# Optimization experiments

Hardware: AMD Instinct MI355X
Metric: run time of the kernel (lower is better)

The kernel has to match this reference:

```python
import jax, jax.numpy as jnp
import numpy as np

# Model constants (from init_kwargs)
NF, NC, E, B = 100000, 4000, 500000, 256
D_FACT, D_COMP = 1536, 27
HIDDEN, HEADS, CPH = 128, 4, 32  # out_per_head = hidden // heads
NUM_LAYERS = 2
TIME_DIM = 8
T_SCALE = 30.0
EDGE_DIM = 2 + TIME_DIM  # [sentiment, decay, time2vec]
ATTN_SCALE = 1.0  # 1 / attn_temperature
NEG_SLOPE = 0.2


def time_edge_features(ea, lam):
    # ea: [E, 2] = [sentiment, decay]; second column in [0,1] -> decay branch
    s = jnp.clip(ea[:, 0:1], -1.0, 1.0)
    decay = jnp.clip(ea[:, 1:2], 0.0, 1.0)
    lam = jnp.maximum(lam, 1e-6)
    delta_t = -jnp.log(jnp.maximum(decay, 1e-6)) / lam
    t = jnp.log1p(jnp.maximum(delta_t, 0.0)) / T_SCALE  # [E,1]
    freqs = jnp.arange(1, TIME_DIM, dtype=ea.dtype)      # [TIME_DIM-1]
    sins = jnp.sin(t * freqs)                            # [E,TIME_DIM-1]
    return jnp.concatenate([s, decay, sins, t], axis=-1)  # [E, EDGE_DIM]


def seg_softmax(logits, seg, n):
    # logits: [E,H]; softmax over edges sharing the same destination node
    m = jax.ops.segment_max(logits, seg, num_segments=n)
    z = jnp.exp(logits - m[seg])
    den = jax.ops.segment_sum(z, seg, num_segments=n)
    return z / (den[seg] + 1e-16)


def seg_mean(x, seg, n):
    s = jax.ops.segment_sum(x, seg, num_segments=n)
    cnt = jax.ops.segment_sum(jnp.ones((x.shape[0],), x.dtype), seg, num_segments=n)
    return s / jnp.maximum(cnt, 1.0)[:, None]


def layernorm(x, g, b, eps=1e-5):
    mu = jnp.mean(x, axis=-1, keepdims=True)
    var = jnp.var(x, axis=-1, keepdims=True)
    return (x - mu) * jax.lax.rsqrt(var + eps) * g + b


def setup_inputs() -> dict:
    key = jax.random.key(0)
    ks = jax.random.split(key, 32)

    x_fact = jax.random.normal(ks[0], (NF, D_FACT), jnp.float32)
    x_company = jax.random.normal(ks[1], (NC, D_COMP), jnp.float32)
    u = jax.random.uniform(ks[2], (E, 2), jnp.float32)
    edge_attr = jnp.concatenate([u[:, 0:1] * 2.0 - 1.0, u[:, 1:2]], axis=1)
    edge_index = jnp.stack([
        jax.random.randint(ks[3], (E,), 0, NF),
        jax.random.randint(ks[4], (E,), 0, NC),
    ]).astype(jnp.int32)
    batch_fact = jnp.sort(jax.random.randint(ks[5], (NF,), 0, B)).astype(jnp.int32)
    batch_company = jnp.sort(jax.random.randint(ks[6], (NC,), 0, B)).astype(jnp.int32)

    def p(k, shape):
        return jax.random.normal(k, shape, jnp.float32) * 0.05

    inp = dict(
        x_fact=x_fact, x_company=x_company, edge_attr=edge_attr,
        edge_index=edge_index, batch_fact=batch_fact, batch_company=batch_company,
        lambda_decay=jnp.array(0.01, jnp.float32),
        Wf=p(ks[7], (D_FACT, HIDDEN)), bf=jnp.zeros((HIDDEN,), jnp.float32),
        Wc=p(ks[8], (D_COMP, HIDDEN)), bc=jnp.zeros((HIDDEN,), jnp.float32),
        Wl=p(ks[9], (NUM_LAYERS, HIDDEN, HIDDEN)), bl=jnp.zeros((NUM_LAYERS, HIDDEN), jnp.float32),
        Wr=p(ks[10], (NUM_LAYERS, HIDDEN, HIDDEN)), br=jnp.zeros((NUM_LAYERS, HIDDEN), jnp.float32),
        We=p(ks[11], (NUM_LAYERS, EDGE_DIM, HIDDEN)), be=jnp.zeros((NUM_LAYERS, HIDDEN), jnp.float32),
        att=p(ks[12], (NUM_LAYERS, HEADS, CPH)),
        bias_out=jnp.zeros((NUM_LAYERS, HIDDEN), jnp.float32),
        ln_g=jnp.ones((NUM_LAYERS, HIDDEN), jnp.float32), ln_b=jnp.zeros((NUM_LAYERS, HIDDEN), jnp.float32),
        Wg=p(ks[13], (2 * HIDDEN, 1)), bg=jnp.zeros((1,), jnp.float32),
        W1=p(ks[14], (HIDDEN, HIDDEN)), b1=jnp.zeros((HIDDEN,), jnp.float32),
        W2=p(ks[15], (HIDDEN, 1)), b2=jnp.zeros((1,), jnp.float32),
    )
    return inp


def reference(x_fact, x_company, edge_attr, edge_index, batch_fact, batch_company,
              lambda_decay, Wf, bf, Wc, bc, Wl, bl, Wr, br, We, be, att, bias_out,
              ln_g, ln_b, Wg, bg, W1, b1, W2, b2):
    src, dst = edge_index[0], edge_index[1]
    ef = time_edge_features(edge_attr, lambda_decay)          # [E, EDGE_DIM]

    # per-node-type input encoders
    hf = jax.nn.relu(x_fact @ Wf + bf)                         # [NF, H]
    hc = jax.nn.relu(x_company @ Wc + bc)                      # [NC, H]
    n_c = x_company.shape[0]

    for l in range(NUM_LAYERS):
        # GATv2 (edge-conditioned, bipartite fact->company, share_weights=False)
        gl = (hf @ Wl[l] + bl[l]).reshape(-1, HEADS, CPH)      # src transform [NF,H,C]
        gr = (hc @ Wr[l] + br[l]).reshape(-1, HEADS, CPH)      # dst transform [NC,H,C]
        ge = (ef @ We[l] + be[l]).reshape(-1, HEADS, CPH)      # edge transform [E,H,C]
        e = jax.nn.leaky_relu(gl[src] + gr[dst] + ge, NEG_SLOPE)  # [E,H,C]
        logits = jnp.einsum('ehc,hc->eh', e, att[l]) * ATTN_SCALE  # [E,H]
        alpha = seg_softmax(logits, dst, n_c)                   # scatter-softmax over dst
        msg = alpha[..., None] * gl[src]                        # [E,H,C]
        out = jax.ops.segment_sum(msg, dst, num_segments=n_c).reshape(n_c, HIDDEN) + bias_out[l]
        hc = layernorm(hc + jax.nn.relu(out), ln_g[l], ln_b[l])  # residual + post-norm

    # gated readout over graphs in batch
    pf = seg_mean(hf, batch_fact, B)                            # [B,H]
    pc = seg_mean(hc, batch_company, B)                         # [B,H]
    g = jax.nn.sigmoid(jnp.concatenate([pf, pc], axis=-1) @ Wg + bg)  # [B,1]
    h = g * pf + (1.0 - g) * pc                                 # [B,H]
    logit = jax.nn.relu(h @ W1 + b1) @ W2 + b2                  # [B,1]
    return logit
```

## Files before the change

### kernel.cpp

```cpp
#include <hip/hip_runtime.h>
#include <hip/hip_bf16.h>
#include <math.h>

#define NFAC 100000
#define NCOMP 4000
#define NEDGE 500000
#define NB 256
#define DF 1536
#define DC 27
#define H 128
#define EDIM 10
#define EDIMP 16

typedef __attribute__((ext_vector_type(8))) short short8v;
typedef __attribute__((ext_vector_type(4))) float f32x4;

#define GLOAD_LDS16(g, l)                                                              \
  __builtin_amdgcn_global_load_lds((const __attribute__((address_space(1))) unsigned int*)(g), \
                                   (__attribute__((address_space(3))) unsigned int*)(l), 16, 0, 0)

__device__ __forceinline__ float group32_sum(float v) {
#pragma unroll
  for (int m = 16; m > 0; m >>= 1) v += __shfl_xor(v, m);
  return v;
}

__device__ __forceinline__ unsigned short bf16rn(float x) {
  unsigned int u = __float_as_uint(x);
  unsigned int r = (u + 0x7fffu + ((u >> 16) & 1u)) >> 16;
  return (unsigned short)r;
}
__device__ __forceinline__ float bf16tof(unsigned short h) {
  return __uint_as_float(((unsigned int)h) << 16);
}

__global__ void k_edge_feat(const float* __restrict__ ea, const float* __restrict__ lamp,
                            float* __restrict__ ef) {
  int e = blockIdx.x * blockDim.x + threadIdx.x;
  if (e >= NEDGE) return;
  float s   = fminf(fmaxf(ea[2 * e], -1.f), 1.f);
  float dec = fminf(fmaxf(ea[2 * e + 1], 0.f), 1.f);
  float lam = fmaxf(lamp[0], 1e-6f);
  float dt  = -logf(fmaxf(dec, 1e-6f)) / lam;
  float t   = log1pf(fmaxf(dt, 0.f)) * (1.f / 30.f);
  float* o = ef + (size_t)e * EDIMP;
  o[0] = s;
  o[1] = dec;
#pragma unroll
  for (int k = 1; k < 8; k++) o[1 + k] = __sinf(t * (float)k);
  o[9] = t;
  o[10] = 0.f; o[11] = 0.f; o[12] = 0.f; o[13] = 0.f; o[14] = 0.f; o[15] = 0.f;
}

__global__ void k_hist(const int* __restrict__ dst, int* __restrict__ deg) {
  int e = blockIdx.x * blockDim.x + threadIdx.x;
  if (e < NEDGE) atomicAdd(&deg[dst[e]], 1);
}

__global__ __launch_bounds__(1024) void k_scan(const int* __restrict__ deg, int* __restrict__ off) {
  __shared__ int s[4096];
  int t = threadIdx.x;
  for (int i = t; i < 4096; i += 1024) s[i] = (i < NCOMP) ? deg[i] : 0;
  __syncthreads();
  for (int d = 1; d < 4096; d <<= 1) {
    int vals[4];
#pragma unroll
    for (int j = 0; j < 4; j++) {
      int i = t + j * 1024;
      vals[j] = (i >= d) ? s[i - d] : 0;
    }
    __syncthreads();
#pragma unroll
    for (int j = 0; j < 4; j++) {
      int i = t + j * 1024;
      s[i] += vals[j];
    }
    __syncthreads();
  }
  for (int i = t; i < 4096; i += 1024) off[i + 1] = s[i];
  if (t == 0) off[0] = 0;
}

__global__ void k_scatter(const int* __restrict__ dst, const int* __restrict__ src,
                          const int* __restrict__ off, int* __restrict__ cur,
                          int* __restrict__ eid, int* __restrict__ srcs) {
  int e = blockIdx.x * blockDim.x + threadIdx.x;
  if (e < NEDGE) {
    int d = dst[e];
    int p = atomicAdd(&cur[d], 1);
    eid[off[d] + p] = e;
    srcs[off[d] + p] = src[e];
  }
}

__global__ void k_conv_w(const float* __restrict__ W, unsigned short* __restrict__ Bh,
                         unsigned short* __restrict__ Bl, int K) {
  int i = blockIdx.x * blockDim.x + threadIdx.x;
  if (i >= K * H) return;
  int k = i >> 7, c = i & 127;
  float x = W[i];
  unsigned short h = bf16rn(x);
  unsigned short l = bf16rn(x - bf16tof(h));
  Bh[(size_t)c * K + k] = h;
  Bl[(size_t)c * K + k] = l;
}

__device__ __forceinline__ unsigned int packhi(unsigned int u1, unsigned int u0) {
  return __builtin_amdgcn_perm(u1, u0, 0x07060302u);
}

__global__ __launch_bounds__(256, 2) void k_gemm_mfma(const float* __restrict__ A,
                                                      const unsigned short* __restrict__ Bth,
                                                      const unsigned short* __restrict__ Btl,
                                                      const float* __restrict__ bias,
                                                      float* __restrict__ C, int M, int K,
                                                      int dorelu, float* __restrict__ Cpart) {
  __shared__ __align__(16) char smem[2][32768];
  int tid = threadIdx.x;
  int wave = tid >> 6, lane = tid & 63;
  int m0 = blockIdx.x * 128;
  int wm = (wave >> 1) * 64, wn = (wave & 1) * 64;
  int fr = lane & 15, fg = lane >> 4;
  int nsplit = gridDim.y;
  int Ks = K / nsplit;
  int kbeg = blockIdx.y * Ks;
  int nIter = Ks >> 5;

  f32x4 acc[4][4];
#pragma unroll
  for (int i = 0; i < 4; i++)
#pragma unroll
    for (int j = 0; j < 4; j++) acc[i][j] = (f32x4){0.f, 0.f, 0.f, 0.f};

  int a_row = (lane >> 3);
  int a_s = lane & 7;
  int b_col = (lane >> 2);
  int b_s = lane & 3;

  auto stage = [&](int buf, int k0) {
    char* base = smem[buf];
#pragma unroll
    for (int q = 0; q < 4; q++) {
      int j = wave + 4 * q;
      int row = j * 8 + a_row;
      int grow = m0 + row;
      if (grow >= M) grow = 0;
      const float* src = A + (size_t)grow * K + k0 + ((a_s ^ (row & 7)) << 2);
      GLOAD_LDS16(src, base + j * 1024);
    }
#pragma unroll
    for (int q = 0; q < 2; q++) {
      int j = wave + 4 * q;
      int col = j * 16 + b_col;
      int soff = k0 + ((b_s ^ (col & 3)) << 3);
      GLOAD_LDS16(Bth + (size_t)col * K + soff, base + 16384 + j * 1024);
      GLOAD_LDS16(Btl + (size_t)col * K + soff, base + 24576 + j * 1024);
    }
  };

  stage(0, kbeg);
  __syncthreads();

  for (int it = 0; it < nIter; ++it) {
    int cur = it & 1;
    if (it + 1 < nIter) stage(cur ^ 1, kbeg + ((it + 1) << 5));
    const char* cb = smem[cur];
    short8v ah[4], al[4];
#pragma unroll
    for (int mf = 0; mf < 4; mf++) {
      int r = wm + 16 * mf + fr;
      int s0 = (2 * fg) ^ (r & 7);
      int s1 = (2 * fg + 1) ^ (r & 7);
      float4 a0 = *(const float4*)(cb + r * 128 + s0 * 16);
      float4 a1 = *(const float4*)(cb + r * 128 + s1 * 16);
      float xs[8] = {a0.x, a0.y, a0.z, a0.w, a1.x, a1.y, a1.z, a1.w};
      unsigned int hu[8], lu[8];
#pragma unroll
      for (int j = 0; j < 8; j++) {
        unsigned int u = __float_as_uint(xs[j]);
        hu[j] = u & 0xffff0000u;
        lu[j] = __float_as_uint(xs[j] - __uint_as_float(hu[j]));
      }
      unsigned int hw[4], lw[4];
#pragma unroll
      for (int j = 0; j < 4; j++) {
        hw[j] = packhi(hu[2 * j + 1], hu[2 * j]);
        lw[j] = packhi(lu[2 * j + 1], lu[2 * j]);
      }
      ah[mf] = *(short8v*)hw;
      al[mf] = *(short8v*)lw;
    }
#pragma unroll
    for (int nf = 0; nf < 4; nf++) {
      int c = wn + 16 * nf + fr;
      int sb = fg ^ (c & 3);
      short8v bh = *(const short8v*)(cb + 16384 + c * 64 + sb * 16);
      short8v bl = *(const short8v*)(cb + 24576 + c * 64 + sb * 16);
#pragma unroll
      for (int mf = 0; mf < 4; mf++) {
        acc[mf][nf] = __builtin_amdgcn_mfma_f32_16x16x32_bf16(ah[mf], bh, acc[mf][nf], 0, 0, 0);
        acc[mf][nf] = __builtin_amdgcn_mfma_f32_16x16x32_bf16(ah[mf], bl, acc[mf][nf], 0, 0, 0);
        acc[mf][nf] = __builtin_amdgcn_mfma_f32_16x16x32_bf16(al[mf], bh, acc[mf][nf], 0, 0, 0);
      }
    }
    __syncthreads();
  }

  if (nsplit == 1) {
#pragma unroll
    for (int mf = 0; mf < 4; mf++) {
      int rbase = m0 + wm + 16 * mf + 4 * fg;
#pragma unroll
      for (int nf = 0; nf < 4; nf++) {
        int col = wn + 16 * nf + fr;
        float bv = bias[col];
#pragma unroll
        for (int j = 0; j < 4; j++) {
          int row = rbase + j;
          if (row < M) {
            float v = acc[mf][nf][j] + bv;
            if (dorelu) v = fmaxf(v, 0.f);
            C[(size_t)row * H + col] = v;
          }
        }
      }
    }
  } else {
    float* P = Cpart + (size_t)blockIdx.y * M * H;
#pragma unroll
    for (int mf = 0; mf < 4; mf++) {
      int rbase = m0 + wm + 16 * mf + 4 * fg;
#pragma unroll
      for (int nf = 0; nf < 4; nf++) {
        int col = wn + 16 * nf + fr;
#pragma unroll
        for (int j = 0; j < 4; j++) {
          int row = rbase + j;
          if (row < M) P[(size_t)row * H + col] = acc[mf][nf][j];
        }
      }
    }
  }
}

__global__ __launch_bounds__(256) void k_reduce2(const float* __restrict__ P0,
                                                 const float* __restrict__ P1,
                                                 const float* __restrict__ bias,
                                                 float* __restrict__ C, int total4) {
  int i = blockIdx.x * blockDim.x + threadIdx.x;
  if (i >= total4) return;
  float4 a = ((const float4*)P0)[i];
  float4 b = ((const float4*)P1)[i];
  float4 bv = ((const float4*)bias)[i & 31];
  float4 r;
  r.x = fmaxf(a.x + b.x + bv.x, 0.f);
  r.y = fmaxf(a.y + b.y + bv.y, 0.f);
  r.z = fmaxf(a.z + b.z + bv.z, 0.f);
  r.w = fmaxf(a.w + b.w + bv.w, 0.f);
  ((float4*)C)[i] = r;
}

__global__ void k_enc_comp(const float* __restrict__ X, const float* __restrict__ Wc,
                           const float* __restrict__ bc, float* __restrict__ hc) {
  int tid = threadIdx.x;
  int r = blockIdx.x * 2 + (tid >> 7);
  int j = tid & 127;
  if (r >= NCOMP) return;
  float acc = bc[j];
  const float* x = X + (size_t)r * DC;
#pragma unroll
  for (int k = 0; k < DC; k++) acc = fmaf(x[k], Wc[k * H + j], acc);
  hc[(size_t)r * H + j] = fmaxf(acc, 0.f);
}

__global__ __launch_bounds__(128) void k_node(
    const float* __restrict__ gl, const float* __restrict__ ef, const int* __restrict__ srcs,
    const int* __restrict__ csr_off, const int* __restrict__ csr_eid,
    const float* __restrict__ Wr, const float* __restrict__ br, const float* __restrict__ We,
    const float* __restrict__ be, const float* __restrict__ att,
    const float* __restrict__ bias_out, const float* __restrict__ lng,
    const float* __restrict__ lnb, float* __restrict__ hc) {
  int v = blockIdx.x;
  int t = threadIdx.x;
  __shared__ float hcs[H];
  __shared__ float red[2], redq[2];
  float x = hc[(size_t)v * H + t];
  hcs[t] = x;
  float wre[EDIM];
#pragma unroll
  for (int k = 0; k < EDIM; k++) wre[k] = We[k * H + t];
  float attv = att[t];
  float bev = be[t];
  __syncthreads();
  float grv = br[t];
  for (int k = 0; k < H; k++) grv = fmaf(hcs[k], Wr[k * H + t], grv);
  float grb = grv + bev;

  int e0 = csr_off[v], e1 = csr_off[v + 1];
  float m = -INFINITY, s = 0.f, acc = 0.f;
  int i = e0;
  int eid = 0, sid = 0;
  if (i < e1) {
    eid = csr_eid[i];
    sid = srcs[i];
  }
  while (i < e1) {
    float glv = gl[(size_t)sid * H + t];
    const float* efr = ef + (size_t)eid * EDIMP;
    float4 f0 = *(const float4*)(efr);
    float4 f1 = *(const float4*)(efr + 4);
    float2 f2 = *(const float2*)(efr + 8);
    int ni = i + 1;
    if (ni < e1) {
      eid = csr_eid[ni];
      sid = srcs[ni];
    }
    float ge = grb;
    ge = fmaf(f0.x, wre[0], ge);
    ge = fmaf(f0.y, wre[1], ge);
    ge = fmaf(f0.z, wre[2], ge);
    ge = fmaf(f0.w, wre[3], ge);
    ge = fmaf(f1.x, wre[4], ge);
    ge = fmaf(f1.y, wre[5], ge);
    ge = fmaf(f1.z, wre[6], ge);
    ge = fmaf(f1.w, wre[7], ge);
    ge = fmaf(f2.x, wre[8], ge);
    ge = fmaf(f2.y, wre[9], ge);
    float ev = glv + ge;
    ev = ev > 0.f ? ev : 0.2f * ev;
    float logit = group32_sum(ev * attv);
    if (logit > m) {
      float scale = __expf(m - logit);
      s = s * scale + 1.f;
      acc = acc * scale + glv;
      m = logit;
    } else {
      float z = __expf(logit - m);
      s += z;
      acc = fmaf(z, glv, acc);
    }
    i = ni;
  }
  float outv = acc / (s + 1e-16f);
  outv += bias_out[t];
  outv = fmaxf(outv, 0.f);
  float y = x + outv;
  float sv = y, qv = y * y;
#pragma unroll
  for (int mm = 32; mm > 0; mm >>= 1) {
    sv += __shfl_xor(sv, mm);
    qv += __shfl_xor(qv, mm);
  }
  int wid = t >> 6, lane = t & 63;
  if (lane == 0) {
    red[wid] = sv;
    redq[wid] = qv;
  }
  __syncthreads();
  float mean = (red[0] + red[1]) * (1.f / H);
  float var = (redq[0] + redq[1]) * (1.f / H) - mean * mean;
  float r = rsqrtf(var + 1e-5f);
  hc[(size_t)v * H + t] = (y - mean) * r * lng[t] + lnb[t];
}

template <int CHUNK>
__global__ __launch_bounds__(128) void k_segmean(const float* __restrict__ X,
                                                 const int* __restrict__ seg, int n,
                                                 float* __restrict__ sum, int* __restrict__ cnt) {
  int t = threadIdx.x;
  int n0 = blockIdx.x * CHUNK;
  int n1 = min(n0 + CHUNK, n);
  float acc = 0.f;
  int c = 0;
  int curs = -1;
  for (int i = n0; i < n1; ++i) {
    int sg = seg[i];
    if (sg != curs) {
      if (curs >= 0) {
        atomicAdd(&sum[(size_t)curs * H + t], acc);
        if (t == 0) atomicAdd(&cnt[curs], c);
      }
      curs = sg;
      acc = 0.f;
      c = 0;
    }
    acc += X[(size_t)i * H + t];
    c++;
  }
  if (curs >= 0) {
    atomicAdd(&sum[(size_t)curs * H + t], acc);
    if (t == 0) atomicAdd(&cnt[curs], c);
  }
}

__global__ __launch_bounds__(128) void k_readout(const float* __restrict__ pf,
                                                 const float* __restrict__ pc,
                                                 const int* __restrict__ cf,
                                                 const int* __restrict__ cc,
                                                 const float* __restrict__ Wg,
                                                 const float* __restrict__ bg,
                                                 const float* __restrict__ W1,
                                                 const float* __restrict__ b1,
                                                 const float* __restrict__ W2,
                                                 const float* __restrict__ b2,
                                                 float* __restrict__ out) {
  int b = blockIdx.x, t = threadIdx.x;
  __shared__ float hs[H];
  __shared__ float red[2], red2[2];
  int wid = t >> 6, lane = t & 63;
  float nf = fmaxf((float)cf[b], 1.f);
  float nc = fmaxf((float)cc[b], 1.f);
  float pfv = pf[(size_t)b * H + t] / nf;
  float pcv = pc[(size_t)b * H + t] / nc;
  float gp = pfv * Wg[t] + pcv * Wg[H + t];
  float sv = gp;
#pragma unroll
  for (int mm = 32; mm > 0; mm >>= 1) sv += __shfl_xor(sv, mm);
  if (lane == 0) red[wid] = sv;
  __syncthreads();
  float g = 1.f / (1.f + expf(-(red[0] + red[1] + bg[0])));
  float h = g * pfv + (1.f - g) * pcv;
  hs[t] = h;
  __syncthreads();
  float a = b1[t];
  for (int k = 0; k < H; k++) a = fmaf(hs[k], W1[k * H + t], a);
  a = fmaxf(a, 0.f);
  float p = a * W2[t];
#pragma unroll
  for (int mm = 32; mm > 0; mm >>= 1) p += __shfl_xor(p, mm);
  if (lane == 0) red2[wid] = p;
  __syncthreads();
  if (t == 0) out[b] = red2[0] + red2[1] + b2[0];
}

extern "C" void kernel_launch(void* const* d_in, const int* in_sizes, int n_in, void* d_out,
                              int out_size, void* d_ws, size_t ws_size, hipStream_t stream) {
  const float* x_fact = (const float*)d_in[0];
  const float* x_comp = (const float*)d_in[1];
  const float* ea = (const float*)d_in[2];
  const int* eidx = (const int*)d_in[3];
  const int* batf = (const int*)d_in[4];
  const int* batc = (const int*)d_in[5];
  const float* lam = (const float*)d_in[6];
  const float* Wf = (const float*)d_in[7];
  const float* bf = (const float*)d_in[8];
  const float* Wc = (const float*)d_in[9];
  const float* bc = (const float*)d_in[10];
  const float* Wl = (const float*)d_in[11];
  const float* bl = (const float*)d_in[12];
  const float* Wr = (const float*)d_in[13];
  const float* br_ = (const float*)d_in[14];
  const float* We = (const float*)d_in[15];
  const float* be = (const float*)d_in[16];
  const float* att = (const float*)d_in[17];
  const float* b_out = (const float*)d_in[18];
  const float* lng = (const float*)d_in[19];
  const float* lnb = (const float*)d_in[20];
  const float* Wg = (const float*)d_in[21];
  const float* bg = (const float*)d_in[22];
  const float* W1 = (const float*)d_in[23];
  const float* b1 = (const float*)d_in[24];
  const float* W2 = (const float*)d_in[25];
  const float* b2 = (const float*)d_in[26];
  float* out = (float*)d_out;

  char* w = (char*)d_ws;
  auto carve = [&](size_t bytes) -> char* {
    char* p = w;
    w += (bytes + 255) & ~(size_t)255;
    return p;
  };
  float* HF = (float*)carve((size_t)NFAC * H * 4);
  float* GL = (float*)carve((size_t)NFAC * H * 4);
  float* CP1 = (float*)carve((size_t)NFAC * H * 4);
  float* HC = (float*)carve((size_t)NCOMP * H * 4);
  float* EF = (float*)carve((size_t)NEDGE * EDIMP * 4);
  int* OFF = (int*)carve(4100 * 4);
  int* EID = (int*)carve((size_t)NEDGE * 4);
  int* SRCS = (int*)carve((size_t)NEDGE * 4);
  unsigned short* WfH = (unsigned short*)carve((size_t)DF * H * 2);
  unsigned short* WfL = (unsigned short*)carve((size_t)DF * H * 2);
  unsigned short* WlH[2], *WlL[2];
  for (int l = 0; l < 2; l++) {
    WlH[l] = (unsigned short*)carve((size_t)H * H * 2);
    WlL[l] = (unsigned short*)carve((size_t)H * H * 2);
  }
  char* zbase = w;
  int* DEG = (int*)carve(4096 * 4);
  int* CUR = (int*)carve(4096 * 4);
  float* PF = (float*)carve((size_t)NB * H * 4);
  float* PC = (float*)carve((size_t)NB * H * 4);
  int* CF = (int*)carve(NB * 4);
  int* CC = (int*)carve(NB * 4);
  size_t zbytes = (size_t)(w - zbase);
  hipMemsetAsync(zbase, 0, zbytes, stream);

  const int* srcArr = eidx;
  const int* dstArr = eidx + NEDGE;

  k_edge_feat<<<(NEDGE + 255) / 256, 256, 0, stream>>>(ea, lam, EF);
  k_hist<<<(NEDGE + 255) / 256, 256, 0, stream>>>(dstArr, DEG);
  k_scan<<<1, 1024, 0, stream>>>(DEG, OFF);
  k_scatter<<<(NEDGE + 255) / 256, 256, 0, stream>>>(dstArr, srcArr, OFF, CUR, EID, SRCS);

  k_conv_w<<<(DF * H + 255) / 256, 256, 0, stream>>>(Wf, WfH, WfL, DF);
  for (int l = 0; l < 2; l++)
    k_conv_w<<<(H * H + 255) / 256, 256, 0, stream>>>(Wl + (size_t)l * H * H, WlH[l], WlL[l], H);

  {
    float* CPART = GL;
    dim3 grid((NFAC + 127) / 128, 2);
    k_gemm_mfma<<<grid, 256, 0, stream>>>(x_fact, WfH, WfL, bf, HF, NFAC, DF, 1, CPART);
    int total4 = NFAC * H / 4;
    k_reduce2<<<(total4 + 255) / 256, 256, 0, stream>>>(GL, CP1, bf, HF, total4);
  }
  k_enc_comp<<<NCOMP / 2, 256, 0, stream>>>(x_comp, Wc, bc, HC);

  for (int l = 0; l < 2; l++) {
    dim3 grid((NFAC + 127) / 128, 1);
    k_gemm_mfma<<<grid, 256, 0, stream>>>(HF, WlH[l], WlL[l], bl + l * H, GL, NFAC, H, 0,
                                          (float*)nullptr);
    k_node<<<NCOMP, 128, 0, stream>>>(GL, EF, SRCS, OFF, EID, Wr + (size_t)l * H * H,
                                      br_ + l * H, We + (size_t)l * EDIM * H, be + l * H,
                                      att + l * H, b_out + l * H, lng + l * H, lnb + l * H, HC);
  }

  k_segmean<128><<<(NFAC + 127) / 128, 128, 0, stream>>>(HF, batf, NFAC, PF, CF);
  k_segmean<64><<<(NCOMP + 63) / 64, 128, 0, stream>>>(HC, batc, NCOMP, PC, CC);
  k_readout<<<NB, 128, 0, stream>>>(PF, PC, CF, CC, Wg, bg, W1, b1, W2, b2, out);
}
```

Before: 707.8 us.

## Batch both layer projections into one N=256 GEMM and prefetch edge data

The fact-node features do not change across layers, so both layers' source projections are computed in one GEMM with N=256. The two Wl matrices are concatenated into a single bf16 hi/lo weight buffer. This reads HF once and saves a launch, and the k_node kernels read their half through a row stride of 256. k_node also gains a software prefetch: the next edge's gl row and edge features are loaded before the current edge is processed, hiding gather latency at the cost of extra registers. The 256-wide output buffer overruns GL into the adjacent CP1 region, which is reused because CP1 is dead by then.

```diff
diff --git a/kernel.cpp b/kernel.cpp
--- a/kernel.cpp
+++ b/kernel.cpp
@@ -105,8 +105,43 @@
   Bl[(size_t)c * K + k] = l;
 }
 
+__global__ void k_conv_wl2(const float* __restrict__ Wl, unsigned short* __restrict__ Bh,
+                           unsigned short* __restrict__ Bl) {
+  int i = blockIdx.x * blockDim.x + threadIdx.x;
+  if (i >= 2 * H * H) return;
+  int l = i >> 14;
+  int r = i & 16383;
+  int k = r >> 7, c = r & 127;
+  float x = Wl[i];
+  unsigned short h = bf16rn(x);
+  unsigned short lo = bf16rn(x - bf16tof(h));
+  int col = c + 128 * l;
+  Bh[(size_t)col * H + k] = h;
+  Bl[(size_t)col * H + k] = lo;
+}
+
 __device__ __forceinline__ unsigned int packhi(unsigned int u1, unsigned int u0) {
   return __builtin_amdgcn_perm(u1, u0, 0x07060302u);
+}
+
+__device__ __forceinline__ void split8(const float4& a0, const float4& a1, short8v& ah,
+                                       short8v& al) {
+  float xs[8] = {a0.x, a0.y, a0.z, a0.w, a1.x, a1.y, a1.z, a1.w};
+  unsigned int hu[8], lu[8];
+#pragma unroll
+  for (int j = 0; j < 8; j++) {
+    unsigned int u = __float_as_uint(xs[j]);
+    hu[j] = u & 0xffff0000u;
+    lu[j] = __float_as_uint(xs[j] - __uint_as_float(hu[j]));
+  }
+  unsigned int hw[4], lw[4];
+#pragma unroll
+  for (int j = 0; j < 4; j++) {
+    hw[j] = packhi(hu[2 * j + 1], hu[2 * j]);
+    lw[j] = packhi(lu[2 * j + 1], lu[2 * j]);
+  }
+  ah = *(short8v*)hw;
+  al = *(short8v*)lw;
 }
 
 __global__ __launch_bounds__(256, 2) void k_gemm_mfma(const float* __restrict__ A,
@@ -173,22 +208,7 @@
       int s1 = (2 * fg + 1) ^ (r & 7);
       float4 a0 = *(const float4*)(cb + r * 128 + s0 * 16);
       float4 a1 = *(const float4*)(cb + r * 128 + s1 * 16);
-      float xs[8] = {a0.x, a0.y, a0.z, a0.w, a1.x, a1.y, a1.z, a1.w};
-      unsigned int hu[8], lu[8];
-#pragma unroll
-      for (int j = 0; j < 8; j++) {
-        unsigned int u = __float_as_uint(xs[j]);
-        hu[j] = u & 0xffff0000u;
-        lu[j] = __float_as_uint(xs[j] - __uint_as_float(hu[j]));
-      }
-      unsigned int hw[4], lw[4];
-#pragma unroll
-      for (int j = 0; j < 4; j++) {
-        hw[j] = packhi(hu[2 * j + 1], hu[2 * j]);
-        lw[j] = packhi(lu[2 * j + 1], lu[2 * j]);
-      }
-      ah[mf] = *(short8v*)hw;
-      al[mf] = *(short8v*)lw;
+      split8(a0, a1, ah[mf], al[mf]);
     }
 #pragma unroll
     for (int nf = 0; nf < 4; nf++) {
@@ -238,6 +258,99 @@
           int row = rbase + j;
           if (row < M) P[(size_t)row * H + col] = acc[mf][nf][j];
         }
+      }
+    }
+  }
+}
+
+__global__ __launch_bounds__(256, 2) void k_gemm_n256(const float* __restrict__ A,
+                                                      const unsigned short* __restrict__ Bth,
+                                                      const unsigned short* __restrict__ Btl,
+                                                      const float* __restrict__ bias,
+                                                      float* __restrict__ C, int M) {
+  __shared__ __align__(16) char smem[2][40960];
+  const int K = 128;
+  int tid = threadIdx.x;
+  int wave = tid >> 6, lane = tid & 63;
+  int m0 = blockIdx.x * 64;
+  int wn = wave * 64;
+  int fr = lane & 15, fg = lane >> 4;
+
+  f32x4 acc[4][4];
+#pragma unroll
+  for (int i = 0; i < 4; i++)
+#pragma unroll
+    for (int j = 0; j < 4; j++) acc[i][j] = (f32x4){0.f, 0.f, 0.f, 0.f};
+
+  int a_row = (lane >> 3);
+  int a_s = lane & 7;
+  int b_col = (lane >> 2);
+  int b_s = lane & 3;
+
+  auto stage = [&](int buf, int k0) {
+    char* base = smem[buf];
+#pragma unroll
+    for (int q = 0; q < 2; q++) {
+      int j = wave + 4 * q;
+      int row = j * 8 + a_row;
+      int grow = m0 + row;
+      if (grow >= M) grow = 0;
+      GLOAD_LDS16(A + (size_t)grow * K + k0 + ((a_s ^ (row & 7)) << 2), base + j * 1024);
+    }
+#pragma unroll
+    for (int q = 0; q < 4; q++) {
+      int j = wave + 4 * q;
+      int col = j * 16 + b_col;
+      int soff = k0 + ((b_s ^ (col & 3)) << 3);
+      GLOAD_LDS16(Bth + (size_t)col * K + soff, base + 8192 + j * 1024);
+      GLOAD_LDS16(Btl + (size_t)col * K + soff, base + 24576 + j * 1024);
+    }
+  };
+
+  stage(0, 0);
+  __syncthreads();
+
+  for (int it = 0; it < 4; ++it) {
+    int cur = it & 1;
+    if (it + 1 < 4) stage(cur ^ 1, (it + 1) << 5);
+    const char* cb = smem[cur];
+    short8v ah[4], al[4];
+#pragma unroll
+    for (int mf = 0; mf < 4; mf++) {
+      int r = 16 * mf + fr;
+      int s0 = (2 * fg) ^ (r & 7);
+      int s1 = (2 * fg + 1) ^ (r & 7);
+      float4 a0 = *(const float4*)(cb + r * 128 + s0 * 16);
+      float4 a1 = *(const float4*)(cb + r * 128 + s1 * 16);
+      split8(a0, a1, ah[mf], al[mf]);
+    }
+#pragma unroll
+    for (int nf = 0; nf < 4; nf++) {
+      int c = wn + 16 * nf + fr;
+      int sb = fg ^ (c & 3);
+      short8v bh = *(const short8v*)(cb + 8192 + c * 64 + sb * 16);
+      short8v bl = *(const short8v*)(cb + 24576 + c * 64 + sb * 16);
+#pragma unroll
+      for (int mf = 0; mf < 4; mf++) {
+        acc[mf][nf] = __builtin_amdgcn_mfma_f32_16x16x32_bf16(ah[mf], bh, acc[mf][nf], 0, 0, 0);
+        acc[mf][nf] = __builtin_amdgcn_mfma_f32_16x16x32_bf16(ah[mf], bl, acc[mf][nf], 0, 0, 0);
+        acc[mf][nf] = __builtin_amdgcn_mfma_f32_16x16x32_bf16(al[mf], bh, acc[mf][nf], 0, 0, 0);
+      }
+    }
+    __syncthreads();
+  }
+
+#pragma unroll
+  for (int mf = 0; mf < 4; mf++) {
+    int rbase = m0 + 16 * mf + 4 * fg;
+#pragma unroll
+    for (int nf = 0; nf < 4; nf++) {
+      int col = wn + 16 * nf + fr;
+      float bv = bias[col];
+#pragma unroll
+      for (int j = 0; j < 4; j++) {
+        int row = rbase + j;
+        if (row < M) C[(size_t)row * 256 + col] = acc[mf][nf][j] + bv;
       }
     }
   }
@@ -299,21 +412,31 @@
   int e0 = csr_off[v], e1 = csr_off[v + 1];
   float m = -INFINITY, s = 0.f, acc = 0.f;
   int i = e0;
-  int eid = 0, sid = 0;
+  float glv = 0.f;
+  float4 f0 = {0, 0, 0, 0}, f1 = {0, 0, 0, 0};
+  float2 f2 = {0, 0};
   if (i < e1) {
-    eid = csr_eid[i];
-    sid = srcs[i];
+    int eid = csr_eid[i];
+    int sid = srcs[i];
+    glv = gl[(size_t)sid * 256 + t];
+    const float* efr = ef + (size_t)eid * EDIMP;
+    f0 = *(const float4*)(efr);
+    f1 = *(const float4*)(efr + 4);
+    f2 = *(const float2*)(efr + 8);
   }
   while (i < e1) {
-    float glv = gl[(size_t)sid * H + t];
-    const float* efr = ef + (size_t)eid * EDIMP;
-    float4 f0 = *(const float4*)(efr);
-    float4 f1 = *(const float4*)(efr + 4);
-    float2 f2 = *(const float2*)(efr + 8);
     int ni = i + 1;
+    float nglv = 0.f;
+    float4 nf0 = {0, 0, 0, 0}, nf1 = {0, 0, 0, 0};
+    float2 nf2 = {0, 0};
     if (ni < e1) {
-      eid = csr_eid[ni];
-      sid = srcs[ni];
+      int eid = csr_eid[ni];
+      int sid = srcs[ni];
+      nglv = gl[(size_t)sid * 256 + t];
+      const float* efr = ef + (size_t)eid * EDIMP;
+      nf0 = *(const float4*)(efr);
+      nf1 = *(const float4*)(efr + 4);
+      nf2 = *(const float2*)(efr + 8);
     }
     float ge = grb;
     ge = fmaf(f0.x, wre[0], ge);
@@ -339,6 +462,10 @@
       s += z;
       acc = fmaf(z, glv, acc);
     }
+    glv = nglv;
+    f0 = nf0;
+    f1 = nf1;
+    f2 = nf2;
     i = ni;
   }
   float outv = acc / (s + 1e-16f);
@@ -473,6 +600,7 @@
   float* HF = (float*)carve((size_t)NFAC * H * 4);
   float* GL = (float*)carve((size_t)NFAC * H * 4);
   float* CP1 = (float*)carve((size_t)NFAC * H * 4);
+  float* GL2 = GL;
   float* HC = (float*)carve((size_t)NCOMP * H * 4);
   float* EF = (float*)carve((size_t)NEDGE * EDIMP * 4);
   int* OFF = (int*)carve(4100 * 4);
@@ -480,11 +608,8 @@
   int* SRCS = (int*)carve((size_t)NEDGE * 4);
   unsigned short* WfH = (unsigned short*)carve((size_t)DF * H * 2);
   unsigned short* WfL = (unsigned short*)carve((size_t)DF * H * 2);
-  unsigned short* WlH[2], *WlL[2];
-  for (int l = 0; l < 2; l++) {
-    WlH[l] = (unsigned short*)carve((size_t)H * H * 2);
-    WlL[l] = (unsigned short*)carve((size_t)H * H * 2);
-  }
+  unsigned short* WlH2 = (unsigned short*)carve((size_t)256 * H * 2);
+  unsigned short* WlL2 = (unsigned short*)carve((size_t)256 * H * 2);
   char* zbase = w;
   int* DEG = (int*)carve(4096 * 4);
   int* CUR = (int*)carve(4096 * 4);
@@ -504,8 +629,7 @@
   k_scatter<<<(NEDGE + 255) / 256, 256, 0, stream>>>(dstArr, srcArr, OFF, CUR, EID, SRCS);
 
   k_conv_w<<<(DF * H + 255) / 256, 256, 0, stream>>>(Wf, WfH, WfL, DF);
-  for (int l = 0; l < 2; l++)
-    k_conv_w<<<(H * H + 255) / 256, 256, 0, stream>>>(Wl + (size_t)l * H * H, WlH[l], WlL[l], H);
+  k_conv_wl2<<<(2 * H * H + 255) / 256, 256, 0, stream>>>(Wl, WlH2, WlL2);
 
   {
     float* CPART = GL;
@@ -516,13 +640,13 @@
   }
   k_enc_comp<<<NCOMP / 2, 256, 0, stream>>>(x_comp, Wc, bc, HC);
 
+  k_gemm_n256<<<(NFAC + 63) / 64, 256, 0, stream>>>(HF, WlH2, WlL2, bl, GL2, NFAC);
+
   for (int l = 0; l < 2; l++) {
-    dim3 grid((NFAC + 127) / 128, 1);
-    k_gemm_mfma<<<grid, 256, 0, stream>>>(HF, WlH[l], WlL[l], bl + l * H, GL, NFAC, H, 0,
-                                          (float*)nullptr);
-    k_node<<<NCOMP, 128, 0, stream>>>(GL, EF, SRCS, OFF, EID, Wr + (size_t)l * H * H,
-                                      br_ + l * H, We + (size_t)l * EDIM * H, be + l * H,
-                                      att + l * H, b_out + l * H, lng + l * H, lnb + l * H, HC);
+    k_node<<<NCOMP, 128, 0, stream>>>(GL2 + l * 128, EF, SRCS, OFF, EID,
+                                      Wr + (size_t)l * H * H, br_ + l * H,
+                                      We + (size_t)l * EDIM * H, be + l * H, att + l * H,
+                                      b_out + l * H, lng + l * H, lnb + l * H, HC);
   }
 
   k_segmean<128><<<(NFAC + 127) / 128, 128, 0, stream>>>(HF, batf, NFAC, PF, CF);
```

Result: slower. 734.9 us (+3.8%).
